# Optimization experiments

Hardware: AMD Instinct MI355X
Metric: run time of the kernel (lower is better)

## Reference

```python
import jax, jax.numpy as jnp
import numpy as np
from jax import lax

H = 512  # out_size (hidden)

def lstm_layer(x, W_ih, W_hh, b_ih, b_hh):
    # x: [B, T, F] -> hidden sequence [B, T, H]; matches torch.nn.LSTMCell math
    B = x.shape[0]
    h0 = jnp.zeros((B, H), dtype=x.dtype)
    c0 = jnp.zeros((B, H), dtype=x.dtype)

    def step(carry, x_t):
        h, c = carry
        gates = x_t @ W_ih.T + b_ih + h @ W_hh.T + b_hh  # [B, 4H], gate order i,f,g,o
        i, f, g, o = jnp.split(gates, 4, axis=-1)
        i = jax.nn.sigmoid(i)
        f = jax.nn.sigmoid(f)
        g = jnp.tanh(g)
        o = jax.nn.sigmoid(o)
        c_new = f * c + i * g
        h_new = o * jnp.tanh(c_new)
        return (h_new, c_new), h_new

    xt = jnp.swapaxes(x, 0, 1)  # [T, B, F]
    (_, _), hs = lax.scan(step, (h0, c0), xt)
    return jnp.swapaxes(hs, 0, 1)  # [B, T, H]


def setup_inputs() -> dict:
    key = jax.random.key(0)
    ks = jax.random.split(key, 9)
    B, T, F = 64, 512, 256
    s = 1.0 / np.sqrt(H)  # torch LSTMCell init scale
    inp = {
        "x": jax.random.normal(ks[0], (B, T, F), dtype=jnp.float32),
        "W_ih0": jax.random.uniform(ks[1], (4 * H, F), jnp.float32, -s, s),
        "W_hh0": jax.random.uniform(ks[2], (4 * H, H), jnp.float32, -s, s),
        "b_ih0": jax.random.uniform(ks[3], (4 * H,), jnp.float32, -s, s),
        "b_hh0": jax.random.uniform(ks[4], (4 * H,), jnp.float32, -s, s),
        "W_ih1": jax.random.uniform(ks[5], (4 * H, H), jnp.float32, -s, s),
        "W_hh1": jax.random.uniform(ks[6], (4 * H, H), jnp.float32, -s, s),
        "b_ih1": jax.random.uniform(ks[7], (4 * H,), jnp.float32, -s, s),
        "b_hh1": jax.random.uniform(ks[8], (4 * H,), jnp.float32, -s, s),
    }
    return inp


def reference(x, W_ih0, W_hh0, b_ih0, b_hh0, W_ih1, W_hh1, b_ih1, b_hh1):
    # Layer 0 (in_size -> H), dropout=0.0 is identity; layer 1 (H -> H)
    a = lstm_layer(x, W_ih0, W_hh0, b_ih0, b_hh0)
    a = lstm_layer(a, W_ih1, W_hh1, b_ih1, b_hh1)
    return a  # yhat: [B, T, H]; final_state is (a[:, -1], c_T) in the original
```

## Files before the change

### kernel.cpp

```cpp
#include <hip/hip_runtime.h>
#include <math.h>


#define TT 512
#define FF 256
#define HH 512
#define NB 256

typedef __attribute__((ext_vector_type(4)))  float f32x4;
typedef __attribute__((ext_vector_type(8)))  short short8;
typedef __attribute__((ext_vector_type(16))) short short16;

__device__ __forceinline__ float sigmoidf_(float v){ return 1.0f/(1.0f+__expf(-v)); }

__device__ __forceinline__ unsigned short f2bf(float f){
    unsigned u = __float_as_uint(f);
    u += 0x7FFFu + ((u>>16)&1u);
    return (unsigned short)(u>>16);
}
__device__ __forceinline__ float bf2f(unsigned short h){ return __uint_as_float(((unsigned)h)<<16); }

__device__ __forceinline__ unsigned long long ld8coh(const unsigned* p){
    return __hip_atomic_load((const unsigned long long*)p, __ATOMIC_RELAXED, __HIP_MEMORY_SCOPE_AGENT);
}
__device__ __forceinline__ int ld4coh(const int* p){
    return __hip_atomic_load(p, __ATOMIC_RELAXED, __HIP_MEMORY_SCOPE_AGENT);
}
__device__ __forceinline__ void st4coh(unsigned* p, unsigned v){
    __hip_atomic_store(p, v, __ATOMIC_RELAXED, __HIP_MEMORY_SCOPE_AGENT);
}
__device__ __forceinline__ void stslot(int* p, int v){
    __hip_atomic_store(p, v, __ATOMIC_RELAXED, __HIP_MEMORY_SCOPE_AGENT);
}

union HU { unsigned long long q[4]; short16 v; };

__device__ __forceinline__ void split8(const float* v, short8& h8, short8& l8){
#pragma unroll
    for (int j=0;j<8;++j){
        const unsigned short hh = f2bf(v[j]);
        h8[j] = (short)hh;
        l8[j] = (short)f2bf(v[j]-bf2f(hh));
    }
}

__device__ __forceinline__ void loadsplit(const float* p, short8& h8, short8& l8){
    float v[8];
#pragma unroll
    for (int j=0;j<8;++j) v[j]=p[j];
    split8(v, h8, l8);
}

#define MFMA(a,b,c) __builtin_amdgcn_mfma_f32_16x16x32_bf16((a),(b),(c),0,0,0)

struct SMem { float part[8][16][66]; };

template<int LAYER>
__device__ __forceinline__ void run(
    const float* __restrict__ x,
    const float* __restrict__ WA, const float* __restrict__ WB,
    const float* __restrict__ bi, const float* __restrict__ bh,
    unsigned* __restrict__ hp0, unsigned* __restrict__ hp1,
    float* __restrict__ out, int* __restrict__ slots,
    const int bg, const int tile_u, SMem* sm)
{
    const int tid  = threadIdx.x;
    const int lane = tid & 63;
    const int wv   = __builtin_amdgcn_readfirstlane(tid>>6);
    const int nn   = lane & 15;
    const int quad = lane >> 4;
    const int bglob= bg*16 + nn;

    constexpr int NC = (LAYER==0) ? 3 : 4;
    short8 wHi[4][NC], wLo[4][NC];
#pragma unroll
    for (int nt=0;nt<4;++nt){
        const int jg = ((nn>>2)<<9) + (tile_u<<4) + (nt<<2) + (nn&3);
        if (LAYER==0){
            const float* rA = WA + (size_t)jg*FF;
            const float* rB = WB + (size_t)jg*HH;
            loadsplit(rA + wv*32 + quad*8, wHi[nt][0], wLo[nt][0]);
#pragma unroll
            for (int c=0;c<2;++c)
                loadsplit(rB + (2*wv+c)*32 + quad*8, wHi[nt][1+c], wLo[nt][1+c]);
        } else {
            const float* rw = ((wv<4) ? WA : WB) + (size_t)jg*HH;
#pragma unroll
            for (int c=0;c<4;++c)
                loadsplit(rw + ((wv&3)*4+c)*32 + quad*8, wHi[nt][c], wLo[nt][c]);
        }
    }

    const int b_e = tid>>4, ul = tid&15;
    const int u_e = (tile_u<<4) + ul;
    float br[4]={0.f,0.f,0.f,0.f}; float creg=0.f;
    if (tid<256){
#pragma unroll
        for (int g=0; g<4; ++g) br[g] = bi[(g<<9)+u_e] + bh[(g<<9)+u_e];
    }

    const int myslot = bg*64 + LAYER*32 + tile_u;
    const f32x4 Z = {0.f,0.f,0.f,0.f};

#define CHUNK_H(OCT, SLOT) { \
        const unsigned* p_ = src + ((size_t)((OCT))*64 + bglob)*8; \
        HU u; \
        u.q[0]=ld8coh(p_);   u.q[1]=ld8coh(p_+2); \
        u.q[2]=ld8coh(p_+4); u.q[3]=ld8coh(p_+6); \
        const short8 aH = __builtin_shufflevector(u.v,u.v,0,2,4,6,8,10,12,14); \
        const short8 aL = __builtin_shufflevector(u.v,u.v,1,3,5,7,9,11,13,15); \
        _Pragma("unroll") \
        for (int nt=0;nt<4;++nt){ \
            accH[nt]=MFMA(aH,wHi[nt][(SLOT)],accH[nt]); \
            accM[nt]=MFMA(aH,wLo[nt][(SLOT)],accM[nt]); \
            accM[nt]=MFMA(aL,wHi[nt][(SLOT)],accM[nt]); \
        } }

    for (int s=0; s<=TT; ++s){
        const bool active = LAYER ? (s>0) : (s<TT);
        const int t = LAYER ? (s-1) : s;
        f32x4 accH[4], accM[4];
#pragma unroll
        for (int nt=0;nt<4;++nt){ accH[nt]=Z; accM[nt]=Z; }

        if (LAYER==0 && active){
            const float* p = x + ((size_t)bglob*TT + t)*FF + wv*32 + quad*8;
            float v[8];
            const float4 a0 = *(const float4*)(p);
            const float4 a1 = *(const float4*)(p+4);
            v[0]=a0.x; v[1]=a0.y; v[2]=a0.z; v[3]=a0.w;
            v[4]=a1.x; v[5]=a1.y; v[6]=a1.z; v[7]=a1.w;
            short8 aH, aL; split8(v, aH, aL);
#pragma unroll
            for (int nt=0;nt<4;++nt){
                accH[nt]=MFMA(aH,wHi[nt][0],accH[nt]);
                accM[nt]=MFMA(aH,wLo[nt][0],accM[nt]);
                accM[nt]=MFMA(aL,wHi[nt][0],accM[nt]);
            }
        }

        if (wv==0){
            const int tgt = (LAYER==0 && lane>=32) ? (s-2) : s;
            const int* sp = slots + bg*64 + lane;
            while (!__all(ld4coh(sp) >= tgt)) __builtin_amdgcn_s_sleep(1);
        }
        __syncthreads();

        if (active){
            if (LAYER==0){
                const unsigned* src = hp0 + ((s+3)&3)*32768;
#pragma unroll
                for (int c=0;c<2;++c)
                    CHUNK_H((2*wv+c)*4+quad, 1+c);
            } else {
                const unsigned* src = (wv<4) ? hp0 + ((s+3)&3)*32768
                                             : hp1 + (s&1)*32768;
#pragma unroll
                for (int c=0;c<4;++c)
                    CHUNK_H(((wv&3)*4+c)*4+quad, c);
            }

#pragma unroll
            for (int nt=0;nt<4;++nt)
#pragma unroll
                for (int r=0;r<4;++r)
                    sm->part[wv][quad*4+r][nt*16+nn] = accH[nt][r]+accM[nt][r];
            __syncthreads();
            if (tid<256){
                float pre[4];
#pragma unroll
                for (int g=0; g<4; ++g){
                    const int col = ((ul>>2)<<4) + (g<<2) + (ul&3);
                    float sum = br[g];
#pragma unroll
                    for (int w=0;w<8;++w) sum += sm->part[w][b_e][col];
                    pre[g]=sum;
                }
                const float iv = sigmoidf_(pre[0]);
                const float fv = sigmoidf_(pre[1]);
                const float gv = tanhf(pre[2]);
                const float ov = sigmoidf_(pre[3]);
                creg = fv*creg + iv*gv;
                const float hn = ov * tanhf(creg);
                const unsigned short hh = f2bf(hn);
                const unsigned short hl = f2bf(hn - bf2f(hh));
                const unsigned pk = ((unsigned)hl<<16) | (unsigned)hh;
                const int bge = bg*16 + b_e;
                const int idx = ((u_e>>3)*64 + bge)*8 + (u_e&7);
                if (LAYER==0) st4coh(hp0 + (s&3)*32768 + idx, pk);
                else {
                    st4coh(hp1 + ((s+1)&1)*32768 + idx, pk);
                    out[((size_t)bge*TT + t)*HH + u_e] = hn;
                }
            }
        }

        __syncthreads();
        if (tid==0) stslot(slots + myslot, s+1);
    }
#undef CHUNK_H
}

__global__ void __launch_bounds__(512,1) lstm_persist(
    const float* __restrict__ x,
    const float* __restrict__ Wih0, const float* __restrict__ Whh0,
    const float* __restrict__ bi0,  const float* __restrict__ bh0,
    const float* __restrict__ Wih1, const float* __restrict__ Whh1,
    const float* __restrict__ bi1,  const float* __restrict__ bh1,
    unsigned* hp0, unsigned* hp1, float* out, int* slots)
{
    __shared__ SMem sm;
    const int layer = blockIdx.x>>7, lid = blockIdx.x&127;
    const int bg = lid>>5, tile_u = lid&31;
    if (layer==0) run<0>(x, Wih0, Whh0, bi0, bh0, hp0, hp1, out, slots, bg, tile_u, &sm);
    else          run<1>(x, Wih1, Whh1, bi1, bh1, hp0, hp1, out, slots, bg, tile_u, &sm);
}

extern "C" void kernel_launch(void* const* d_in, const int* in_sizes, int n_in,
                              void* d_out, int out_size, void* d_ws, size_t ws_size,
                              hipStream_t stream) {
    (void)in_sizes; (void)n_in; (void)out_size; (void)ws_size;
    const float* x    = (const float*)d_in[0];
    const float* Wih0 = (const float*)d_in[1];
    const float* Whh0 = (const float*)d_in[2];
    const float* bi0  = (const float*)d_in[3];
    const float* bh0  = (const float*)d_in[4];
    const float* Wih1 = (const float*)d_in[5];
    const float* Whh1 = (const float*)d_in[6];
    const float* bi1  = (const float*)d_in[7];
    const float* bh1  = (const float*)d_in[8];
    float* out = (float*)d_out;
    unsigned* ws = (unsigned*)d_ws;

    unsigned* hp0 = ws;
    unsigned* hp1 = ws + 4*32768;
    int* slots    = (int*)(ws + 6*32768);

    hipMemsetAsync(d_ws, 0, (6*32768 + 256)*sizeof(unsigned), stream);

    void* args[] = {
        (void*)&x, (void*)&Wih0, (void*)&Whh0, (void*)&bi0, (void*)&bh0,
        (void*)&Wih1, (void*)&Whh1, (void*)&bi1, (void*)&bh1,
        (void*)&hp0, (void*)&hp1, (void*)&out, (void*)&slots
    };
    hipLaunchCooperativeKernel((const void*)lstm_persist, dim3(NB), dim3(512),
                               args, 0, stream);
}
```

Baseline: 2.517 ms.

## Split layer-0 spin-wait and batch coherent h loads before MFMAs

Layer 0 now waits only on its own layer's slots before the recurrent matmul. The wait on layer 1's progress (the ring-buffer write-after-read guard) moves to just before the h store, so the matmul overlaps the cross-layer wait. All coherent h loads for a step are also issued before any MFMA work to expose memory-level parallelism. This adds an extra barrier per step and holds more h fragments in registers.

```diff
diff --git a/kernel.cpp b/kernel.cpp
--- a/kernel.cpp
+++ b/kernel.cpp
@@ -102,13 +102,14 @@
     const int myslot = bg*64 + LAYER*32 + tile_u;
     const f32x4 Z = {0.f,0.f,0.f,0.f};
 
-#define CHUNK_H(OCT, SLOT) { \
+#define LOADH(U, OCT) { \
         const unsigned* p_ = src + ((size_t)((OCT))*64 + bglob)*8; \
-        HU u; \
-        u.q[0]=ld8coh(p_);   u.q[1]=ld8coh(p_+2); \
-        u.q[2]=ld8coh(p_+4); u.q[3]=ld8coh(p_+6); \
-        const short8 aH = __builtin_shufflevector(u.v,u.v,0,2,4,6,8,10,12,14); \
-        const short8 aL = __builtin_shufflevector(u.v,u.v,1,3,5,7,9,11,13,15); \
+        U.q[0]=ld8coh(p_);   U.q[1]=ld8coh(p_+2); \
+        U.q[2]=ld8coh(p_+4); U.q[3]=ld8coh(p_+6); }
+
+#define MATHH(U, SLOT) { \
+        const short8 aH = __builtin_shufflevector(U.v,U.v,0,2,4,6,8,10,12,14); \
+        const short8 aL = __builtin_shufflevector(U.v,U.v,1,3,5,7,9,11,13,15); \
         _Pragma("unroll") \
         for (int nt=0;nt<4;++nt){ \
             accH[nt]=MFMA(aH,wHi[nt][(SLOT)],accH[nt]); \
@@ -140,24 +141,32 @@
         }
 
         if (wv==0){
-            const int tgt = (LAYER==0 && lane>=32) ? (s-2) : s;
-            const int* sp = slots + bg*64 + lane;
-            while (!__all(ld4coh(sp) >= tgt)) __builtin_amdgcn_s_sleep(1);
+            if (LAYER==0){
+                const int* sp = slots + bg*64 + (lane&31);
+                while (!__all(ld4coh(sp) >= s)) __builtin_amdgcn_s_sleep(1);
+            } else {
+                const int* sp = slots + bg*64 + lane;
+                while (!__all(ld4coh(sp) >= s)) __builtin_amdgcn_s_sleep(1);
+            }
         }
         __syncthreads();
 
         if (active){
             if (LAYER==0){
                 const unsigned* src = hp0 + ((s+3)&3)*32768;
-#pragma unroll
-                for (int c=0;c<2;++c)
-                    CHUNK_H((2*wv+c)*4+quad, 1+c);
+                HU u0,u1;
+                LOADH(u0,(2*wv+0)*4+quad);
+                LOADH(u1,(2*wv+1)*4+quad);
+                MATHH(u0,1); MATHH(u1,2);
             } else {
                 const unsigned* src = (wv<4) ? hp0 + ((s+3)&3)*32768
                                              : hp1 + (s&1)*32768;
-#pragma unroll
-                for (int c=0;c<4;++c)
-                    CHUNK_H(((wv&3)*4+c)*4+quad, c);
+                HU u0,u1,u2,u3;
+                LOADH(u0,((wv&3)*4+0)*4+quad);
+                LOADH(u1,((wv&3)*4+1)*4+quad);
+                LOADH(u2,((wv&3)*4+2)*4+quad);
+                LOADH(u3,((wv&3)*4+3)*4+quad);
+                MATHH(u0,0); MATHH(u1,1); MATHH(u2,2); MATHH(u3,3);
             }
 
 #pragma unroll
@@ -165,40 +174,47 @@
 #pragma unroll
                 for (int r=0;r<4;++r)
                     sm->part[wv][quad*4+r][nt*16+nn] = accH[nt][r]+accM[nt][r];
-            __syncthreads();
-            if (tid<256){
-                float pre[4];
-#pragma unroll
-                for (int g=0; g<4; ++g){
-                    const int col = ((ul>>2)<<4) + (g<<2) + (ul&3);
-                    float sum = br[g];
-#pragma unroll
-                    for (int w=0;w<8;++w) sum += sm->part[w][b_e][col];
-                    pre[g]=sum;
-                }
-                const float iv = sigmoidf_(pre[0]);
-                const float fv = sigmoidf_(pre[1]);
-                const float gv = tanhf(pre[2]);
-                const float ov = sigmoidf_(pre[3]);
-                creg = fv*creg + iv*gv;
-                const float hn = ov * tanhf(creg);
-                const unsigned short hh = f2bf(hn);
-                const unsigned short hl = f2bf(hn - bf2f(hh));
-                const unsigned pk = ((unsigned)hl<<16) | (unsigned)hh;
-                const int bge = bg*16 + b_e;
-                const int idx = ((u_e>>3)*64 + bge)*8 + (u_e&7);
-                if (LAYER==0) st4coh(hp0 + (s&3)*32768 + idx, pk);
-                else {
-                    st4coh(hp1 + ((s+1)&1)*32768 + idx, pk);
-                    out[((size_t)bge*TT + t)*HH + u_e] = hn;
-                }
+        }
+
+        if (LAYER==0 && wv==0){
+            const int* sp2 = slots + bg*64 + 32 + (lane&31);
+            while (!__all(ld4coh(sp2) >= s-2)) __builtin_amdgcn_s_sleep(1);
+        }
+        __syncthreads();
+
+        if (active && tid<256){
+            float pre[4];
+#pragma unroll
+            for (int g=0; g<4; ++g){
+                const int col = ((ul>>2)<<4) + (g<<2) + (ul&3);
+                float sum = br[g];
+#pragma unroll
+                for (int w=0;w<8;++w) sum += sm->part[w][b_e][col];
+                pre[g]=sum;
+            }
+            const float iv = sigmoidf_(pre[0]);
+            const float fv = sigmoidf_(pre[1]);
+            const float gv = tanhf(pre[2]);
+            const float ov = sigmoidf_(pre[3]);
+            creg = fv*creg + iv*gv;
+            const float hn = ov * tanhf(creg);
+            const unsigned short hh = f2bf(hn);
+            const unsigned short hl = f2bf(hn - bf2f(hh));
+            const unsigned pk = ((unsigned)hl<<16) | (unsigned)hh;
+            const int bge = bg*16 + b_e;
+            const int idx = ((u_e>>3)*64 + bge)*8 + (u_e&7);
+            if (LAYER==0) st4coh(hp0 + (s&3)*32768 + idx, pk);
+            else {
+                st4coh(hp1 + ((s+1)&1)*32768 + idx, pk);
+                out[((size_t)bge*TT + t)*HH + u_e] = hn;
             }
         }
 
         __syncthreads();
         if (tid==0) stslot(slots + myslot, s+1);
     }
-#undef CHUNK_H
+#undef LOADH
+#undef MATHH
 }
 
 __global__ void __launch_bounds__(512,1) lstm_persist(
```

Measured after the change: 2.459 ms. 1.02x faster.
